# Kernel tuning notes

Hardware: AMD Instinct MI355X
Metric: run time of the kernel (lower is better)

Reference implementation:

```python
import jax, jax.numpy as jnp
import numpy as np

B, N, K, D = 2, 4096, 20, 128
PH = 8          # pos_mlp hidden dim
AH = 4 * D      # attn_mlp hidden dim (attn_mlp_hidden_mult=4)


def setup_inputs() -> dict:
    key = jax.random.key(0)
    ks = jax.random.split(key, 12)
    s = 0.02
    f32 = jnp.float32
    return {
        "x": jax.random.normal(ks[0], (B, N, 3), f32),
        "pos": jax.random.normal(ks[1], (B, N, 3), f32),
        # linear1/2/3 (torch Linear: y = x @ W.T + b)
        "W1": jax.random.normal(ks[2], (D, 3), f32) * s,  "b1": jnp.zeros((D,), f32),
        "W2": jax.random.normal(ks[3], (D, D), f32) * s,  "b2": jnp.zeros((D,), f32),
        "W3": jax.random.normal(ks[4], (D, D), f32) * s,  "b3": jnp.zeros((D,), f32),
        # PointTransformerLayer params
        "Wqkv": jax.random.normal(ks[5], (3 * D, D), f32) * s,          # to_qkv, no bias
        "Wp1": jax.random.normal(ks[6], (PH, 3), f32) * s,  "bp1": jnp.zeros((PH,), f32),
        "Wp2": jax.random.normal(ks[7], (D, PH), f32) * s,  "bp2": jnp.zeros((D,), f32),
        "Wa1": jax.random.normal(ks[8], (AH, D), f32) * s,  "ba1": jnp.zeros((AH,), f32),
        "Wa2": jax.random.normal(ks[9], (D, AH), f32) * s,  "ba2": jnp.zeros((D,), f32),
    }


def reference(x, pos, W1, b1, W2, b2, W3, b3, Wqkv,
              Wp1, bp1, Wp2, bp2, Wa1, ba1, Wa2, ba2):
    h = x @ W1.T + b1            # [B,N,D] linear1
    h1 = h @ W2.T + b2           # [B,N,D] linear2

    # --- PointTransformerLayer (lucidrains, KNN vector attention) ---
    qkv = h1 @ Wqkv.T            # [B,N,3D]
    q, k, v = jnp.split(qkv, 3, axis=-1)

    # squared pairwise distances and K nearest neighbors (self included)
    d2 = jnp.sum((pos[:, :, None, :] - pos[:, None, :, :]) ** 2, axis=-1)  # [B,N,N]
    _, idx = jax.lax.top_k(-d2, K)                                          # [B,N,K]

    gather = jax.vmap(lambda arr, ind: arr[ind])  # per-batch gather -> [B,N,K,*]
    kn = gather(k, idx)          # [B,N,K,D]
    vn = gather(v, idx)          # [B,N,K,D]
    pn = gather(pos, idx)        # [B,N,K,3]

    rel = pos[:, :, None, :] - pn                                   # [B,N,K,3]
    pe = jax.nn.relu(rel @ Wp1.T + bp1) @ Wp2.T + bp2               # pos_mlp [B,N,K,D]

    vn = vn + pe
    sim = jax.nn.relu((q[:, :, None, :] - kn + pe) @ Wa1.T + ba1) @ Wa2.T + ba2  # attn_mlp
    attn = jax.nn.softmax(sim, axis=2)                              # softmax over neighbors
    agg = jnp.sum(attn * vn, axis=2)                                # [B,N,D]

    return h + (agg @ W3.T + b3)  # residual: x + linear3(x1)
```

## Files before the change

kernel.cpp:

```cpp
#include <hip/hip_runtime.h>
#include <stdint.h>

#define BB 2
#define NN 4096
#define KNB 20
#define DD 128
#define PHH 8
#define AHH 512
#define BN (BB*NN)

typedef unsigned short ushort_t;
typedef short bf16x8 __attribute__((ext_vector_type(8)));
typedef float f32x4 __attribute__((ext_vector_type(4)));

__device__ __forceinline__ uint32_t umin32(uint32_t a, uint32_t b) { return a < b ? a : b; }
__device__ __forceinline__ uint32_t umax32(uint32_t a, uint32_t b) { return a > b ? a : b; }

__device__ __forceinline__ ushort_t f2bf(float f) {
    uint32_t x = __float_as_uint(f);
    return (ushort_t)((x + 0x7FFFu + ((x >> 16) & 1u)) >> 16);
}
__device__ __forceinline__ float bf2f(ushort_t u) {
    union { float f; uint32_t i; } c; c.i = ((uint32_t)u) << 16; return c.f;
}

#define SW256(m, byteInRow) ((m)*256 + ((byteInRow) ^ (((m)&7) << 4)))
#define SW128(m, byteInRow) ((m)*128 + ((byteInRow) ^ (((m)&7) << 4)))

__global__ __launch_bounds__(256) void k_prep(
        const float* __restrict__ Wa1, const float* __restrict__ Wa2,
        const float* __restrict__ W2, const float* __restrict__ Wqkv,
        const float* __restrict__ W3, ushort_t* __restrict__ wbf) {
    int i = blockIdx.x*256 + threadIdx.x;
    float v;
    if (i < 65536)        v = Wa1[i];
    else if (i < 131072)  v = Wa2[i - 65536];
    else if (i < 147456)  v = W2[i - 131072];
    else if (i < 196608)  v = Wqkv[i - 147456];
    else                  v = W3[i - 196608];
    wbf[i] = f2bf(v);
}

__global__ __launch_bounds__(256) void k_front(
        const float* __restrict__ x,
        const float* __restrict__ W1, const float* __restrict__ b1,
        const ushort_t* __restrict__ W2bf, const float* __restrict__ b2,
        const ushort_t* __restrict__ Wqkvbf,
        float* __restrict__ h, ushort_t* __restrict__ qf,
        ushort_t* __restrict__ kf, ushort_t* __restrict__ vf) {
    __shared__ __align__(16) char smem[16896];
    float* xs = (float*)(smem + 16384);
    int tid = threadIdx.x, w = tid >> 6, lane = tid & 63;
    int p0 = blockIdx.x * 32;

    if (tid < 96) xs[tid] = x[(size_t)p0*3 + tid];
    __syncthreads();

    #pragma unroll
    for (int it = 0; it < 16; ++it) {
        int lin = it*256 + tid;
        int m = lin >> 7, d = lin & 127;
        float hv = b1[d] + xs[m*3+0]*W1[d*3+0] + xs[m*3+1]*W1[d*3+1] + xs[m*3+2]*W1[d*3+2];
        h[(size_t)(p0+m)*DD + d] = hv;
        *(ushort_t*)&smem[SW256(m, d*2)] = f2bf(hv);
    }
    __syncthreads();

    {
        f32x4 acc[2][2];
        #pragma unroll
        for (int mt = 0; mt < 2; ++mt)
            #pragma unroll
            for (int ntl = 0; ntl < 2; ++ntl) acc[mt][ntl] = (f32x4){0,0,0,0};
        #pragma unroll
        for (int ks = 0; ks < 4; ++ks) {
            int k0 = ks*32 + (lane >> 4)*8;
            bf16x8 aF[2];
            #pragma unroll
            for (int mt = 0; mt < 2; ++mt)
                aF[mt] = *(const bf16x8*)&smem[SW256(mt*16 + (lane & 15), k0*2)];
            #pragma unroll
            for (int ntl = 0; ntl < 2; ++ntl) {
                int n = (2*w + ntl)*16 + (lane & 15);
                bf16x8 bF = *(const bf16x8*)&W2bf[(size_t)n*DD + k0];
                #pragma unroll
                for (int mt = 0; mt < 2; ++mt)
                    acc[mt][ntl] = __builtin_amdgcn_mfma_f32_16x16x32_bf16(aF[mt], bF, acc[mt][ntl], 0, 0, 0);
            }
        }
        #pragma unroll
        for (int ntl = 0; ntl < 2; ++ntl) {
            int n = (2*w + ntl)*16 + (lane & 15);
            float bias = b2[n];
            #pragma unroll
            for (int mt = 0; mt < 2; ++mt)
                #pragma unroll
                for (int i = 0; i < 4; ++i) {
                    int m = mt*16 + (lane >> 4)*4 + i;
                    *(ushort_t*)&smem[8192 + SW256(m, n*2)] = f2bf(acc[mt][ntl][i] + bias);
                }
        }
    }
    __syncthreads();

    {
        f32x4 acc[2][6];
        #pragma unroll
        for (int mt = 0; mt < 2; ++mt)
            #pragma unroll
            for (int ntl = 0; ntl < 6; ++ntl) acc[mt][ntl] = (f32x4){0,0,0,0};
        #pragma unroll
        for (int ks = 0; ks < 4; ++ks) {
            int k0 = ks*32 + (lane >> 4)*8;
            bf16x8 aF[2];
            #pragma unroll
            for (int mt = 0; mt < 2; ++mt)
                aF[mt] = *(const bf16x8*)&smem[8192 + SW256(mt*16 + (lane & 15), k0*2)];
            #pragma unroll
            for (int ntl = 0; ntl < 6; ++ntl) {
                int n = (w*6 + ntl)*16 + (lane & 15);
                bf16x8 bF = *(const bf16x8*)&Wqkvbf[(size_t)n*DD + k0];
                #pragma unroll
                for (int mt = 0; mt < 2; ++mt)
                    acc[mt][ntl] = __builtin_amdgcn_mfma_f32_16x16x32_bf16(aF[mt], bF, acc[mt][ntl], 0, 0, 0);
            }
        }
        #pragma unroll
        for (int ntl = 0; ntl < 6; ++ntl) {
            int n = (w*6 + ntl)*16 + (lane & 15);
            int r = n >> 7, d = n & 127;
            ushort_t* dst = (r == 0) ? qf : (r == 1) ? kf : vf;
            #pragma unroll
            for (int mt = 0; mt < 2; ++mt)
                #pragma unroll
                for (int i = 0; i < 4; ++i) {
                    int m = mt*16 + (lane >> 4)*4 + i;
                    dst[(size_t)(p0+m)*DD + d] = f2bf(acc[mt][ntl][i]);
                }
        }
    }
}

__global__ __launch_bounds__(256) void k_knn(const float* __restrict__ pos, int* __restrict__ idx) {
    int wid  = threadIdx.x >> 6;
    int lane = threadIdx.x & 63;
    int p = blockIdx.x*4 + wid;
    int b = p >> 12;
    float qx = pos[p*3+0], qy = pos[p*3+1], qz = pos[p*3+2];
    const float* pb = pos + (size_t)b*NN*3;

    uint32_t bk[KNB];
    #pragma unroll
    for (int i = 0; i < KNB; ++i) bk[i] = 0xFFFFFFFFu;

    for (int i = 0; i < NN/64; ++i) {
        int j = i*64 + lane;
        float dx = qx - pb[j*3+0];
        float dy = qy - pb[j*3+1];
        float dz = qz - pb[j*3+2];
        float d2 = dx*dx + dy*dy + dz*dz;
        uint32_t key = (__float_as_uint(d2) & 0xFFFFF000u) | (uint32_t)j;
        if (key < bk[KNB-1]) {
            uint32_t c = key;
            #pragma unroll
            for (int t = 0; t < KNB; ++t) {
                uint32_t lo = umin32(c, bk[t]);
                uint32_t hi = umax32(c, bk[t]);
                bk[t] = lo; c = hi;
            }
        }
    }
    for (int r = 0; r < KNB; ++r) {
        uint32_t m = bk[0];
        #pragma unroll
        for (int s = 1; s < 64; s <<= 1)
            m = umin32(m, (uint32_t)__shfl_xor((int)m, s, 64));
        if (lane == 0) idx[(size_t)p*KNB + r] = (int)(m & 0xFFFu);
        bool win = (bk[0] == m);
        #pragma unroll
        for (int t = 0; t < KNB-1; ++t) bk[t] = win ? bk[t+1] : bk[t];
        bk[KNB-1] = win ? 0xFFFFFFFFu : bk[KNB-1];
    }
}

#define XL_OFF 0
#define TL_OFF 20480
#define PH_OFF 30720
#define NIDX_OFF 33280
#define SIM_STRIDE 272

__global__ __launch_bounds__(256, 4) void k_attn(
        const float* __restrict__ pos,
        const ushort_t* __restrict__ qf, const ushort_t* __restrict__ kf,
        const ushort_t* __restrict__ vf, const int* __restrict__ idx,
        const float* __restrict__ Wp1, const float* __restrict__ bp1,
        const float* __restrict__ Wp2, const float* __restrict__ bp2,
        const ushort_t* __restrict__ Wa1bf, const float* __restrict__ ba1,
        const ushort_t* __restrict__ Wa2bf, const float* __restrict__ ba2,
        float* __restrict__ agg) {
    __shared__ __align__(16) char smem[33600];
    float* phv  = (float*)(smem + PH_OFF);
    int*   nidx = (int*)(smem + NIDX_OFF);

    int tid = threadIdx.x, w = tid >> 6, lane = tid & 63;
    int p0 = blockIdx.x * 4, b = p0 >> 12;

    if (tid < 80) nidx[tid] = idx[(size_t)(p0 + tid/20)*KNB + (tid%20)];
    __syncthreads();

    for (int lin = tid; lin < 80*PHH; lin += 256) {
        int m = lin >> 3, jj = lin & 7;
        int g = m / 20;
        int j = nidx[m];
        const float* pq = pos + (size_t)(p0 + g)*3;
        const float* pn = pos + (size_t)(b*NN + j)*3;
        float r0 = pq[0]-pn[0], r1 = pq[1]-pn[1], r2 = pq[2]-pn[2];
        float a = bp1[jj] + r0*Wp1[jj*3+0] + r1*Wp1[jj*3+1] + r2*Wp1[jj*3+2];
        phv[m*PHH + jj] = fmaxf(a, 0.f);
    }
    __syncthreads();

    {
        int d = tid & 127;
        int mpar = tid >> 7;
        float4 wp2a = *(const float4*)(Wp2 + (size_t)d*PHH);
        float4 wp2b = *(const float4*)(Wp2 + (size_t)d*PHH + 4);
        float bp2d = bp2[d];
        float qv[4];
        #pragma unroll
        for (int g = 0; g < 4; ++g) qv[g] = bf2f(qf[(size_t)(p0+g)*DD + d]);
        #pragma unroll
        for (int g = 0; g < 4; ++g) {
            #pragma unroll
            for (int t = 0; t < 10; ++t) {
                int m = g*20 + mpar + 2*t;
                int j = nidx[m];
                float4 pa = *(const float4*)(phv + m*PHH);
                float4 pb = *(const float4*)(phv + m*PHH + 4);
                float pe = bp2d + pa.x*wp2a.x + pa.y*wp2a.y + pa.z*wp2a.z + pa.w*wp2a.w
                                + pb.x*wp2b.x + pb.y*wp2b.y + pb.z*wp2b.z + pb.w*wp2b.w;
                float kv = bf2f(kf[(size_t)(b*NN + j)*DD + d]);
                *(ushort_t*)&smem[XL_OFF + SW256(m, d*2)] = f2bf(qv[g] - kv + pe);
            }
        }
    }
    __syncthreads();

    f32x4 accS[5][2];
    #pragma unroll
    for (int mt = 0; mt < 5; ++mt)
        #pragma unroll
        for (int ntl = 0; ntl < 2; ++ntl) accS[mt][ntl] = (f32x4){0,0,0,0};

    for (int c = 0; c < 8; ++c) {
        f32x4 accB[5];
        #pragma unroll
        for (int mt = 0; mt < 5; ++mt) accB[mt] = (f32x4){0,0,0,0};
        #pragma unroll
        for (int ks = 0; ks < 4; ++ks) {
            int k0 = ks*32 + (lane >> 4)*8;
            bf16x8 aF[5];
            #pragma unroll
            for (int mt = 0; mt < 5; ++mt)
                aF[mt] = *(const bf16x8*)&smem[XL_OFF + SW256(mt*16 + (lane & 15), k0*2)];
            bf16x8 bF = *(const bf16x8*)&Wa1bf[(size_t)(c*64 + w*16 + (lane & 15))*DD + k0];
            #pragma unroll
            for (int mt = 0; mt < 5; ++mt)
                accB[mt] = __builtin_amdgcn_mfma_f32_16x16x32_bf16(aF[mt], bF, accB[mt], 0, 0, 0);
        }
        {
            int al = w*16 + (lane & 15);
            float bias = ba1[c*64 + al];
            #pragma unroll
            for (int mt = 0; mt < 5; ++mt)
                #pragma unroll
                for (int i = 0; i < 4; ++i) {
                    int m = mt*16 + (lane >> 4)*4 + i;
                    *(ushort_t*)&smem[TL_OFF + SW128(m, al*2)] = f2bf(fmaxf(accB[mt][i] + bias, 0.f));
                }
        }
        __syncthreads();

        #pragma unroll
        for (int ks = 0; ks < 2; ++ks) {
            int k0 = ks*32 + (lane >> 4)*8;
            bf16x8 aF[5];
            #pragma unroll
            for (int mt = 0; mt < 5; ++mt)
                aF[mt] = *(const bf16x8*)&smem[TL_OFF + SW128(mt*16 + (lane & 15), k0*2)];
            #pragma unroll
            for (int ntl = 0; ntl < 2; ++ntl) {
                int dd = w*32 + ntl*16 + (lane & 15);
                bf16x8 bF = *(const bf16x8*)&Wa2bf[(size_t)dd*AHH + c*64 + k0];
                #pragma unroll
                for (int mt = 0; mt < 5; ++mt)
                    accS[mt][ntl] = __builtin_amdgcn_mfma_f32_16x16x32_bf16(aF[mt], bF, accS[mt][ntl], 0, 0, 0);
            }
        }
        __syncthreads();
    }

    #pragma unroll
    for (int ntl = 0; ntl < 2; ++ntl) {
        int dd = w*32 + ntl*16 + (lane & 15);
        float bias2 = ba2[dd];
        #pragma unroll
        for (int mt = 0; mt < 5; ++mt)
            #pragma unroll
            for (int i = 0; i < 4; ++i) {
                int m = mt*16 + (lane >> 4)*4 + i;
                *(ushort_t*)&smem[m*SIM_STRIDE + dd*2] = f2bf(accS[mt][ntl][i] + bias2);
            }
    }
    __syncthreads();

    {
        int d = tid & 127;
        int g2 = tid >> 7;
        float4 wp2a = *(const float4*)(Wp2 + (size_t)d*PHH);
        float4 wp2b = *(const float4*)(Wp2 + (size_t)d*PHH + 4);
        float bp2d = bp2[d];
        #pragma unroll
        for (int gi = 0; gi < 2; ++gi) {
            int g = g2 + gi*2;
            float s = 0.f, anum = 0.f;
            #pragma unroll
            for (int kk = 0; kk < KNB; ++kk) {
                int m = g*20 + kk;
                int j = nidx[m];
                float sim = bf2f(*(const ushort_t*)&smem[m*SIM_STRIDE + d*2]);
                float4 pa = *(const float4*)(phv + m*PHH);
                float4 pb = *(const float4*)(phv + m*PHH + 4);
                float pe = bp2d + pa.x*wp2a.x + pa.y*wp2a.y + pa.z*wp2a.z + pa.w*wp2a.w
                                + pb.x*wp2b.x + pb.y*wp2b.y + pb.z*wp2b.z + pb.w*wp2b.w;
                float vv = bf2f(vf[(size_t)(b*NN + j)*DD + d]);
                float e = __expf(sim);
                anum += e * (vv + pe);
                s += e;
            }
            agg[(size_t)(p0 + g)*DD + d] = anum / s;
        }
    }
}

__global__ __launch_bounds__(256) void k_out(
        const float* __restrict__ agg, const float* __restrict__ h,
        const ushort_t* __restrict__ W3bf, const float* __restrict__ b3,
        float* __restrict__ out) {
    __shared__ __align__(16) char smem[8192];
    int tid = threadIdx.x, w = tid >> 6, lane = tid & 63;
    int p0 = blockIdx.x * 32;

    #pragma unroll
    for (int it = 0; it < 16; ++it) {
        int lin = it*256 + tid;
        int m = lin >> 7, d = lin & 127;
        *(ushort_t*)&smem[SW256(m, d*2)] = f2bf(agg[(size_t)(p0+m)*DD + d]);
    }
    __syncthreads();

    f32x4 acc[2][2];
    #pragma unroll
    for (int mt = 0; mt < 2; ++mt)
        #pragma unroll
        for (int ntl = 0; ntl < 2; ++ntl) acc[mt][ntl] = (f32x4){0,0,0,0};
    #pragma unroll
    for (int ks = 0; ks < 4; ++ks) {
        int k0 = ks*32 + (lane >> 4)*8;
        bf16x8 aF[2];
        #pragma unroll
        for (int mt = 0; mt < 2; ++mt)
            aF[mt] = *(const bf16x8*)&smem[SW256(mt*16 + (lane & 15), k0*2)];
        #pragma unroll
        for (int ntl = 0; ntl < 2; ++ntl) {
            int n = (2*w + ntl)*16 + (lane & 15);
            bf16x8 bF = *(const bf16x8*)&W3bf[(size_t)n*DD + k0];
            #pragma unroll
            for (int mt = 0; mt < 2; ++mt)
                acc[mt][ntl] = __builtin_amdgcn_mfma_f32_16x16x32_bf16(aF[mt], bF, acc[mt][ntl], 0, 0, 0);
        }
    }
    #pragma unroll
    for (int ntl = 0; ntl < 2; ++ntl) {
        int n = (2*w + ntl)*16 + (lane & 15);
        float bias = b3[n];
        #pragma unroll
        for (int mt = 0; mt < 2; ++mt)
            #pragma unroll
            for (int i = 0; i < 4; ++i) {
                int m = mt*16 + (lane >> 4)*4 + i;
                size_t o = (size_t)(p0+m)*DD + n;
                out[o] = acc[mt][ntl][i] + bias + h[o];
            }
    }
}

extern "C" void kernel_launch(void* const* d_in, const int* in_sizes, int n_in,
                              void* d_out, int out_size, void* d_ws, size_t ws_size,
                              hipStream_t stream) {
    const float* x    = (const float*)d_in[0];
    const float* pos  = (const float*)d_in[1];
    const float* W1   = (const float*)d_in[2];
    const float* b1   = (const float*)d_in[3];
    const float* W2   = (const float*)d_in[4];
    const float* b2   = (const float*)d_in[5];
    const float* W3   = (const float*)d_in[6];
    const float* b3   = (const float*)d_in[7];
    const float* Wqkv = (const float*)d_in[8];
    const float* Wp1  = (const float*)d_in[9];
    const float* bp1  = (const float*)d_in[10];
    const float* Wp2  = (const float*)d_in[11];
    const float* bp2  = (const float*)d_in[12];
    const float* Wa1  = (const float*)d_in[13];
    const float* ba1  = (const float*)d_in[14];
    const float* Wa2  = (const float*)d_in[15];
    const float* ba2  = (const float*)d_in[16];

    float* ws = (float*)d_ws;
    float* h   = ws;
    float* agg = ws + (size_t)BN*DD;
    ushort_t* qf = (ushort_t*)(ws + 2*(size_t)BN*DD);
    ushort_t* kf = qf + (size_t)BN*DD;
    ushort_t* vf = qf + 2*(size_t)BN*DD;
    int* idx = (int*)((char*)d_ws + 14680064);
    ushort_t* wbf = (ushort_t*)((char*)d_ws + 15335424);
    ushort_t* Wa1bf  = wbf;
    ushort_t* Wa2bf  = wbf + 65536;
    ushort_t* W2bf   = wbf + 131072;
    ushort_t* Wqkvbf = wbf + 147456;
    ushort_t* W3bf   = wbf + 196608;

    k_prep <<<832, 256, 0, stream>>>(Wa1, Wa2, W2, Wqkv, W3, wbf);
    k_front<<<BN/32, 256, 0, stream>>>(x, W1, b1, W2bf, b2, Wqkvbf, h, qf, kf, vf);
    k_knn  <<<BN/4, 256, 0, stream>>>(pos, idx);
    k_attn <<<BN/4, 256, 0, stream>>>(pos, qf, kf, vf, idx,
                                      Wp1, bp1, Wp2, bp2, Wa1bf, ba1, Wa2bf, ba2, agg);
    k_out  <<<BN/32, 256, 0, stream>>>(agg, h, W3bf, b3, (float*)d_out);
}
```

Measured before the change: 179.9 us.

## Merge prep, front and KNN into one launch; restructure attention epilogue with MFMA pos-MLP

Three independent launches (weight cast, front linear layers, KNN) become one kernel that dispatches on block index. Only the large attention weights are still pre-cast to bf16; the small weights are converted on the fly with v_cvt_pk_bf16_f32. In k_attn, the position-MLP second layer now runs on MFMA and v+pe is kept packed in registers. The softmax aggregation is done straight from the MFMA accumulators with cross-lane shuffles, removing the shared-memory sim buffer and an extra barrier. This saves launch gaps and LDS traffic but adds register pressure and bf16 rounding of the positional hidden values.

```diff
diff --git a/kernel.cpp b/kernel.cpp
--- a/kernel.cpp
+++ b/kernel.cpp
@@ -23,171 +23,177 @@
 __device__ __forceinline__ float bf2f(ushort_t u) {
     union { float f; uint32_t i; } c; c.i = ((uint32_t)u) << 16; return c.f;
 }
+__device__ __forceinline__ uint32_t cvt_pk_bf16(float lo, float hi) {
+    uint32_t r;
+    asm("v_cvt_pk_bf16_f32 %0, %1, %2" : "=v"(r) : "v"(lo), "v"(hi));
+    return r;
+}
+__device__ __forceinline__ bf16x8 load_bfrag(const float* __restrict__ src) {
+    float4 x = *(const float4*)src;
+    float4 y = *(const float4*)(src + 4);
+    union { bf16x8 v; uint32_t u[4]; } r;
+    r.u[0] = cvt_pk_bf16(x.x, x.y);
+    r.u[1] = cvt_pk_bf16(x.z, x.w);
+    r.u[2] = cvt_pk_bf16(y.x, y.y);
+    r.u[3] = cvt_pk_bf16(y.z, y.w);
+    return r.v;
+}
 
 #define SW256(m, byteInRow) ((m)*256 + ((byteInRow) ^ (((m)&7) << 4)))
 #define SW128(m, byteInRow) ((m)*128 + ((byteInRow) ^ (((m)&7) << 4)))
 
-__global__ __launch_bounds__(256) void k_prep(
+__global__ __launch_bounds__(256) void k_mega(
+        const float* __restrict__ x, const float* __restrict__ pos,
+        const float* __restrict__ W1, const float* __restrict__ b1,
+        const float* __restrict__ W2f, const float* __restrict__ b2,
+        const float* __restrict__ Wqkvf,
         const float* __restrict__ Wa1, const float* __restrict__ Wa2,
-        const float* __restrict__ W2, const float* __restrict__ Wqkv,
-        const float* __restrict__ W3, ushort_t* __restrict__ wbf) {
-    int i = blockIdx.x*256 + threadIdx.x;
-    float v;
-    if (i < 65536)        v = Wa1[i];
-    else if (i < 131072)  v = Wa2[i - 65536];
-    else if (i < 147456)  v = W2[i - 131072];
-    else if (i < 196608)  v = Wqkv[i - 147456];
-    else                  v = W3[i - 196608];
-    wbf[i] = f2bf(v);
-}
-
-__global__ __launch_bounds__(256) void k_front(
-        const float* __restrict__ x,
-        const float* __restrict__ W1, const float* __restrict__ b1,
-        const ushort_t* __restrict__ W2bf, const float* __restrict__ b2,
-        const ushort_t* __restrict__ Wqkvbf,
         float* __restrict__ h, ushort_t* __restrict__ qf,
-        ushort_t* __restrict__ kf, ushort_t* __restrict__ vf) {
+        ushort_t* __restrict__ kf, ushort_t* __restrict__ vf,
+        int* __restrict__ idx, ushort_t* __restrict__ wbf) {
     __shared__ __align__(16) char smem[16896];
-    float* xs = (float*)(smem + 16384);
     int tid = threadIdx.x, w = tid >> 6, lane = tid & 63;
-    int p0 = blockIdx.x * 32;
-
-    if (tid < 96) xs[tid] = x[(size_t)p0*3 + tid];
-    __syncthreads();
-
-    #pragma unroll
-    for (int it = 0; it < 16; ++it) {
-        int lin = it*256 + tid;
-        int m = lin >> 7, d = lin & 127;
-        float hv = b1[d] + xs[m*3+0]*W1[d*3+0] + xs[m*3+1]*W1[d*3+1] + xs[m*3+2]*W1[d*3+2];
-        h[(size_t)(p0+m)*DD + d] = hv;
-        *(ushort_t*)&smem[SW256(m, d*2)] = f2bf(hv);
-    }
-    __syncthreads();
-
-    {
-        f32x4 acc[2][2];
-        #pragma unroll
-        for (int mt = 0; mt < 2; ++mt)
-            #pragma unroll
-            for (int ntl = 0; ntl < 2; ++ntl) acc[mt][ntl] = (f32x4){0,0,0,0};
-        #pragma unroll
-        for (int ks = 0; ks < 4; ++ks) {
-            int k0 = ks*32 + (lane >> 4)*8;
-            bf16x8 aF[2];
+    int bid = blockIdx.x;
+
+    if (bid < BN/4) {
+        int p = bid*4 + w;
+        int b = p >> 12;
+        float qx = pos[p*3+0], qy = pos[p*3+1], qz = pos[p*3+2];
+        const float* pb = pos + (size_t)b*NN*3;
+        uint32_t bk[KNB];
+        #pragma unroll
+        for (int i = 0; i < KNB; ++i) bk[i] = 0xFFFFFFFFu;
+        for (int i = 0; i < NN/64; ++i) {
+            int j = i*64 + lane;
+            float dx = qx - pb[j*3+0];
+            float dy = qy - pb[j*3+1];
+            float dz = qz - pb[j*3+2];
+            float d2 = dx*dx + dy*dy + dz*dz;
+            uint32_t key = (__float_as_uint(d2) & 0xFFFFF000u) | (uint32_t)j;
+            if (key < bk[KNB-1]) {
+                uint32_t c = key;
+                #pragma unroll
+                for (int t = 0; t < KNB; ++t) {
+                    uint32_t lo = umin32(c, bk[t]);
+                    uint32_t hi = umax32(c, bk[t]);
+                    bk[t] = lo; c = hi;
+                }
+            }
+        }
+        for (int r = 0; r < KNB; ++r) {
+            uint32_t m = bk[0];
+            #pragma unroll
+            for (int s = 1; s < 64; s <<= 1)
+                m = umin32(m, (uint32_t)__shfl_xor((int)m, s, 64));
+            if (lane == 0) idx[(size_t)p*KNB + r] = (int)(m & 0xFFFu);
+            bool win = (bk[0] == m);
+            #pragma unroll
+            for (int t = 0; t < KNB-1; ++t) bk[t] = win ? bk[t+1] : bk[t];
+            bk[KNB-1] = win ? 0xFFFFFFFFu : bk[KNB-1];
+        }
+    } else if (bid < BN/4 + BN/32) {
+        float* xs = (float*)(smem + 16384);
+        int p0 = (bid - BN/4) * 32;
+        if (tid < 96) xs[tid] = x[(size_t)p0*3 + tid];
+        __syncthreads();
+
+        #pragma unroll
+        for (int it = 0; it < 16; ++it) {
+            int lin = it*256 + tid;
+            int m = lin >> 7, d = lin & 127;
+            float hv = b1[d] + xs[m*3+0]*W1[d*3+0] + xs[m*3+1]*W1[d*3+1] + xs[m*3+2]*W1[d*3+2];
+            h[(size_t)(p0+m)*DD + d] = hv;
+            *(ushort_t*)&smem[SW256(m, d*2)] = f2bf(hv);
+        }
+        __syncthreads();
+
+        {
+            f32x4 acc[2][2];
             #pragma unroll
             for (int mt = 0; mt < 2; ++mt)
-                aF[mt] = *(const bf16x8*)&smem[SW256(mt*16 + (lane & 15), k0*2)];
+                #pragma unroll
+                for (int ntl = 0; ntl < 2; ++ntl) acc[mt][ntl] = (f32x4){0,0,0,0};
+            #pragma unroll
+            for (int ks = 0; ks < 4; ++ks) {
+                int k0 = ks*32 + (lane >> 4)*8;
+                bf16x8 aF[2];
+                #pragma unroll
+                for (int mt = 0; mt < 2; ++mt)
+                    aF[mt] = *(const bf16x8*)&smem[SW256(mt*16 + (lane & 15), k0*2)];
+                #pragma unroll
+                for (int ntl = 0; ntl < 2; ++ntl) {
+                    int n = (2*w + ntl)*16 + (lane & 15);
+                    bf16x8 bF = load_bfrag(W2f + (size_t)n*DD + k0);
+                    #pragma unroll
+                    for (int mt = 0; mt < 2; ++mt)
+                        acc[mt][ntl] = __builtin_amdgcn_mfma_f32_16x16x32_bf16(aF[mt], bF, acc[mt][ntl], 0, 0, 0);
+                }
+            }
             #pragma unroll
             for (int ntl = 0; ntl < 2; ++ntl) {
                 int n = (2*w + ntl)*16 + (lane & 15);
-                bf16x8 bF = *(const bf16x8*)&W2bf[(size_t)n*DD + k0];
+                float bias = b2[n];
                 #pragma unroll
                 for (int mt = 0; mt < 2; ++mt)
-                    acc[mt][ntl] = __builtin_amdgcn_mfma_f32_16x16x32_bf16(aF[mt], bF, acc[mt][ntl], 0, 0, 0);
-            }
-        }
-        #pragma unroll
-        for (int ntl = 0; ntl < 2; ++ntl) {
-            int n = (2*w + ntl)*16 + (lane & 15);
-            float bias = b2[n];
+                    #pragma unroll
+                    for (int i = 0; i < 4; ++i) {
+                        int m = mt*16 + (lane >> 4)*4 + i;
+                        *(ushort_t*)&smem[8192 + SW256(m, n*2)] = f2bf(acc[mt][ntl][i] + bias);
+                    }
+            }
+        }
+        __syncthreads();
+
+        {
+            f32x4 acc[2][6];
             #pragma unroll
             for (int mt = 0; mt < 2; ++mt)
                 #pragma unroll
-                for (int i = 0; i < 4; ++i) {
-                    int m = mt*16 + (lane >> 4)*4 + i;
-                    *(ushort_t*)&smem[8192 + SW256(m, n*2)] = f2bf(acc[mt][ntl][i] + bias);
+                for (int ntl = 0; ntl < 6; ++ntl) acc[mt][ntl] = (f32x4){0,0,0,0};
+            #pragma unroll
+            for (int ks = 0; ks < 4; ++ks) {
+                int k0 = ks*32 + (lane >> 4)*8;
+                bf16x8 aF[2];
+                #pragma unroll
+                for (int mt = 0; mt < 2; ++mt)
+                    aF[mt] = *(const bf16x8*)&smem[8192 + SW256(mt*16 + (lane & 15), k0*2)];
+                #pragma unroll
+                for (int ntl = 0; ntl < 6; ++ntl) {
+                    int n = (w*6 + ntl)*16 + (lane & 15);
+                    bf16x8 bF = load_bfrag(Wqkvf + (size_t)n*DD + k0);
+                    #pragma unroll
+                    for (int mt = 0; mt < 2; ++mt)
+                        acc[mt][ntl] = __builtin_amdgcn_mfma_f32_16x16x32_bf16(aF[mt], bF, acc[mt][ntl], 0, 0, 0);
                 }
-        }
-    }
-    __syncthreads();
-
-    {
-        f32x4 acc[2][6];
-        #pragma unroll
-        for (int mt = 0; mt < 2; ++mt)
-            #pragma unroll
-            for (int ntl = 0; ntl < 6; ++ntl) acc[mt][ntl] = (f32x4){0,0,0,0};
-        #pragma unroll
-        for (int ks = 0; ks < 4; ++ks) {
-            int k0 = ks*32 + (lane >> 4)*8;
-            bf16x8 aF[2];
-            #pragma unroll
-            for (int mt = 0; mt < 2; ++mt)
-                aF[mt] = *(const bf16x8*)&smem[8192 + SW256(mt*16 + (lane & 15), k0*2)];
+            }
             #pragma unroll
             for (int ntl = 0; ntl < 6; ++ntl) {
                 int n = (w*6 + ntl)*16 + (lane & 15);
-                bf16x8 bF = *(const bf16x8*)&Wqkvbf[(size_t)n*DD + k0];
+                int r = n >> 7, d = n & 127;
+                ushort_t* dst = (r == 0) ? qf : (r == 1) ? kf : vf;
                 #pragma unroll
                 for (int mt = 0; mt < 2; ++mt)
-                    acc[mt][ntl] = __builtin_amdgcn_mfma_f32_16x16x32_bf16(aF[mt], bF, acc[mt][ntl], 0, 0, 0);
-            }
-        }
-        #pragma unroll
-        for (int ntl = 0; ntl < 6; ++ntl) {
-            int n = (w*6 + ntl)*16 + (lane & 15);
-            int r = n >> 7, d = n & 127;
-            ushort_t* dst = (r == 0) ? qf : (r == 1) ? kf : vf;
-            #pragma unroll
-            for (int mt = 0; mt < 2; ++mt)
-                #pragma unroll
-                for (int i = 0; i < 4; ++i) {
-                    int m = mt*16 + (lane >> 4)*4 + i;
-                    dst[(size_t)(p0+m)*DD + d] = f2bf(acc[mt][ntl][i]);
-                }
-        }
-    }
-}
-
-__global__ __launch_bounds__(256) void k_knn(const float* __restrict__ pos, int* __restrict__ idx) {
-    int wid  = threadIdx.x >> 6;
-    int lane = threadIdx.x & 63;
-    int p = blockIdx.x*4 + wid;
-    int b = p >> 12;
-    float qx = pos[p*3+0], qy = pos[p*3+1], qz = pos[p*3+2];
-    const float* pb = pos + (size_t)b*NN*3;
-
-    uint32_t bk[KNB];
-    #pragma unroll
-    for (int i = 0; i < KNB; ++i) bk[i] = 0xFFFFFFFFu;
-
-    for (int i = 0; i < NN/64; ++i) {
-        int j = i*64 + lane;
-        float dx = qx - pb[j*3+0];
-        float dy = qy - pb[j*3+1];
-        float dz = qz - pb[j*3+2];
-        float d2 = dx*dx + dy*dy + dz*dz;
-        uint32_t key = (__float_as_uint(d2) & 0xFFFFF000u) | (uint32_t)j;
-        if (key < bk[KNB-1]) {
-            uint32_t c = key;
-            #pragma unroll
-            for (int t = 0; t < KNB; ++t) {
-                uint32_t lo = umin32(c, bk[t]);
-                uint32_t hi = umax32(c, bk[t]);
-                bk[t] = lo; c = hi;
-            }
-        }
-    }
-    for (int r = 0; r < KNB; ++r) {
-        uint32_t m = bk[0];
-        #pragma unroll
-        for (int s = 1; s < 64; s <<= 1)
-            m = umin32(m, (uint32_t)__shfl_xor((int)m, s, 64));
-        if (lane == 0) idx[(size_t)p*KNB + r] = (int)(m & 0xFFFu);
-        bool win = (bk[0] == m);
-        #pragma unroll
-        for (int t = 0; t < KNB-1; ++t) bk[t] = win ? bk[t+1] : bk[t];
-        bk[KNB-1] = win ? 0xFFFFFFFFu : bk[KNB-1];
+                    #pragma unroll
+                    for (int i = 0; i < 4; ++i) {
+                        int m = mt*16 + (lane >> 4)*4 + i;
+                        dst[(size_t)(p0+m)*DD + d] = f2bf(acc[mt][ntl][i]);
+                    }
+            }
+        }
+    } else {
+        int base = (bid - (BN/4 + BN/32)) * 2048 + tid * 8;
+        const float* src = (base < 65536) ? (Wa1 + base) : (Wa2 + (base - 65536));
+        union { ushort_t u[8]; uint4 q; } pk;
+        #pragma unroll
+        for (int i = 0; i < 8; ++i) pk.u[i] = f2bf(src[i]);
+        *(uint4*)&wbf[base] = pk.q;
     }
 }
 
 #define XL_OFF 0
 #define TL_OFF 20480
 #define PH_OFF 30720
-#define NIDX_OFF 33280
-#define SIM_STRIDE 272
+#define NIDX_OFF 32000
 
 __global__ __launch_bounds__(256, 4) void k_attn(
         const float* __restrict__ pos,
@@ -198,50 +204,79 @@
         const ushort_t* __restrict__ Wa1bf, const float* __restrict__ ba1,
         const ushort_t* __restrict__ Wa2bf, const float* __restrict__ ba2,
         float* __restrict__ agg) {
-    __shared__ __align__(16) char smem[33600];
-    float* phv  = (float*)(smem + PH_OFF);
-    int*   nidx = (int*)(smem + NIDX_OFF);
+    __shared__ __align__(16) char smem[32320];
+    int* nidx = (int*)(smem + NIDX_OFF);
 
     int tid = threadIdx.x, w = tid >> 6, lane = tid & 63;
+    int lg = lane >> 4, c16 = lane & 15;
     int p0 = blockIdx.x * 4, b = p0 >> 12;
 
     if (tid < 80) nidx[tid] = idx[(size_t)(p0 + tid/20)*KNB + (tid%20)];
     __syncthreads();
 
-    for (int lin = tid; lin < 80*PHH; lin += 256) {
-        int m = lin >> 3, jj = lin & 7;
-        int g = m / 20;
+    if (tid < 80) {
+        int m = tid, g = m / 20;
         int j = nidx[m];
-        const float* pq = pos + (size_t)(p0 + g)*3;
-        const float* pn = pos + (size_t)(b*NN + j)*3;
+        const float* pq = pos + (size_t)(p0+g)*3;
+        const float* pn = pos + (size_t)(b*NN+j)*3;
         float r0 = pq[0]-pn[0], r1 = pq[1]-pn[1], r2 = pq[2]-pn[2];
-        float a = bp1[jj] + r0*Wp1[jj*3+0] + r1*Wp1[jj*3+1] + r2*Wp1[jj*3+2];
-        phv[m*PHH + jj] = fmaxf(a, 0.f);
+        union { ushort_t u[8]; uint4 q; } pk;
+        #pragma unroll
+        for (int jj = 0; jj < PHH; ++jj) {
+            float a = bp1[jj] + r0*Wp1[jj*3+0] + r1*Wp1[jj*3+1] + r2*Wp1[jj*3+2];
+            pk.u[jj] = f2bf(fmaxf(a, 0.f));
+        }
+        *(uint4*)&smem[PH_OFF + m*16] = pk.q;
     }
     __syncthreads();
 
-    {
-        int d = tid & 127;
-        int mpar = tid >> 7;
-        float4 wp2a = *(const float4*)(Wp2 + (size_t)d*PHH);
-        float4 wp2b = *(const float4*)(Wp2 + (size_t)d*PHH + 4);
-        float bp2d = bp2[d];
-        float qv[4];
-        #pragma unroll
-        for (int g = 0; g < 4; ++g) qv[g] = bf2f(qf[(size_t)(p0+g)*DD + d]);
-        #pragma unroll
-        for (int g = 0; g < 4; ++g) {
-            #pragma unroll
-            for (int t = 0; t < 10; ++t) {
-                int m = g*20 + mpar + 2*t;
-                int j = nidx[m];
-                float4 pa = *(const float4*)(phv + m*PHH);
-                float4 pb = *(const float4*)(phv + m*PHH + 4);
-                float pe = bp2d + pa.x*wp2a.x + pa.y*wp2a.y + pa.z*wp2a.z + pa.w*wp2a.w
-                                + pb.x*wp2b.x + pb.y*wp2b.y + pb.z*wp2b.z + pb.w*wp2b.w;
-                float kv = bf2f(kf[(size_t)(b*NN + j)*DD + d]);
-                *(ushort_t*)&smem[XL_OFF + SW256(m, d*2)] = f2bf(qv[g] - kv + pe);
-            }
+    int dA = w*32 + c16, dB = w*32 + 16 + c16;
+    float bp2A = bp2[dA], bp2B = bp2[dB];
+    float ba2A = ba2[dA], ba2B = ba2[dB];
+
+    bf16x8 bP0 = {0,0,0,0,0,0,0,0}, bP1 = {0,0,0,0,0,0,0,0};
+    if (lg == 0) {
+        bP0 = load_bfrag(Wp2 + (size_t)dA*PHH);
+        bP1 = load_bfrag(Wp2 + (size_t)dB*PHH);
+    }
+
+    float qv[4][2];
+    #pragma unroll
+    for (int g = 0; g < 4; ++g) {
+        qv[g][0] = bf2f(qf[(size_t)(p0+g)*DD + dA]);
+        qv[g][1] = bf2f(qf[(size_t)(p0+g)*DD + dB]);
+    }
+
+    uint32_t vpe_pk[5][4];
+
+    #pragma unroll
+    for (int mt = 0; mt < 5; ++mt) {
+        bf16x8 aP = {0,0,0,0,0,0,0,0};
+        if (lg == 0) aP = *(const bf16x8*)&smem[PH_OFF + (mt*16 + c16)*16];
+        f32x4 accP0 = (f32x4){0,0,0,0}, accP1 = (f32x4){0,0,0,0};
+        accP0 = __builtin_amdgcn_mfma_f32_16x16x32_bf16(aP, bP0, accP0, 0, 0, 0);
+        accP1 = __builtin_amdgcn_mfma_f32_16x16x32_bf16(aP, bP1, accP1, 0, 0, 0);
+        float qsA = (mt==0) ? qv[0][0]
+                  : (mt==1) ? (lg>=1 ? qv[1][0] : qv[0][0])
+                  : (mt==2) ? (lg>=2 ? qv[2][0] : qv[1][0])
+                  : (mt==3) ? (lg==3 ? qv[3][0] : qv[2][0])
+                  : qv[3][0];
+        float qsB = (mt==0) ? qv[0][1]
+                  : (mt==1) ? (lg>=1 ? qv[1][1] : qv[0][1])
+                  : (mt==2) ? (lg>=2 ? qv[2][1] : qv[1][1])
+                  : (mt==3) ? (lg==3 ? qv[3][1] : qv[2][1])
+                  : qv[3][1];
+        #pragma unroll
+        for (int i = 0; i < 4; ++i) {
+            int m = mt*16 + lg*4 + i;
+            int j = nidx[m];
+            const ushort_t* kr = kf + (size_t)(b*NN+j)*DD;
+            const ushort_t* vr = vf + (size_t)(b*NN+j)*DD;
+            float peA = accP0[i] + bp2A;
+            float peB = accP1[i] + bp2B;
+            *(ushort_t*)&smem[XL_OFF + SW256(m, dA*2)] = f2bf(qsA - bf2f(kr[dA]) + peA);
+            *(ushort_t*)&smem[XL_OFF + SW256(m, dB*2)] = f2bf(qsB - bf2f(kr[dB]) + peB);
+            vpe_pk[mt][i] = cvt_pk_bf16(bf2f(vr[dA]) + peA, bf2f(vr[dB]) + peB);
         }
     }
     __syncthreads();
@@ -258,24 +293,24 @@
         for (int mt = 0; mt < 5; ++mt) accB[mt] = (f32x4){0,0,0,0};
         #pragma unroll
         for (int ks = 0; ks < 4; ++ks) {
-            int k0 = ks*32 + (lane >> 4)*8;
+            int k0 = ks*32 + lg*8;
             bf16x8 aF[5];
             #pragma unroll
             for (int mt = 0; mt < 5; ++mt)
-                aF[mt] = *(const bf16x8*)&smem[XL_OFF + SW256(mt*16 + (lane & 15), k0*2)];
-            bf16x8 bF = *(const bf16x8*)&Wa1bf[(size_t)(c*64 + w*16 + (lane & 15))*DD + k0];
+                aF[mt] = *(const bf16x8*)&smem[XL_OFF + SW256(mt*16 + c16, k0*2)];
+            bf16x8 bF = *(const bf16x8*)&Wa1bf[(size_t)(c*64 + w*16 + c16)*DD + k0];
             #pragma unroll
             for (int mt = 0; mt < 5; ++mt)
                 accB[mt] = __builtin_amdgcn_mfma_f32_16x16x32_bf16(aF[mt], bF, accB[mt], 0, 0, 0);
         }
         {
-            int al = w*16 + (lane & 15);
+            int al = w*16 + c16;
             float bias = ba1[c*64 + al];
             #pragma unroll
             for (int mt = 0; mt < 5; ++mt)
                 #pragma unroll
                 for (int i = 0; i < 4; ++i) {
-                    int m = mt*16 + (lane >> 4)*4 + i;
+                    int m = mt*16 + lg*4 + i;
                     *(ushort_t*)&smem[TL_OFF + SW128(m, al*2)] = f2bf(fmaxf(accB[mt][i] + bias, 0.f));
                 }
         }
@@ -283,14 +318,14 @@
 
         #pragma unroll
         for (int ks = 0; ks < 2; ++ks) {
-            int k0 = ks*32 + (lane >> 4)*8;
+            int k0 = ks*32 + lg*8;
             bf16x8 aF[5];
             #pragma unroll
             for (int mt = 0; mt < 5; ++mt)
-                aF[mt] = *(const bf16x8*)&smem[TL_OFF + SW128(mt*16 + (lane & 15), k0*2)];
+                aF[mt] = *(const bf16x8*)&smem[TL_OFF + SW128(mt*16 + c16, k0*2)];
             #pragma unroll
             for (int ntl = 0; ntl < 2; ++ntl) {
-                int dd = w*32 + ntl*16 + (lane & 15);
+                int dd = w*32 + ntl*16 + c16;
                 bf16x8 bF = *(const bf16x8*)&Wa2bf[(size_t)dd*AHH + c*64 + k0];
                 #pragma unroll
                 for (int mt = 0; mt < 5; ++mt)
@@ -300,52 +335,58 @@
         __syncthreads();
     }
 
-    #pragma unroll
-    for (int ntl = 0; ntl < 2; ++ntl) {
-        int dd = w*32 + ntl*16 + (lane & 15);
-        float bias2 = ba2[dd];
-        #pragma unroll
-        for (int mt = 0; mt < 5; ++mt)
-            #pragma unroll
-            for (int i = 0; i < 4; ++i) {
-                int m = mt*16 + (lane >> 4)*4 + i;
-                *(ushort_t*)&smem[m*SIM_STRIDE + dd*2] = f2bf(accS[mt][ntl][i] + bias2);
-            }
-    }
-    __syncthreads();
-
-    {
-        int d = tid & 127;
-        int g2 = tid >> 7;
-        float4 wp2a = *(const float4*)(Wp2 + (size_t)d*PHH);
-        float4 wp2b = *(const float4*)(Wp2 + (size_t)d*PHH + 4);
-        float bp2d = bp2[d];
-        #pragma unroll
-        for (int gi = 0; gi < 2; ++gi) {
-            int g = g2 + gi*2;
-            float s = 0.f, anum = 0.f;
-            #pragma unroll
-            for (int kk = 0; kk < KNB; ++kk) {
-                int m = g*20 + kk;
-                int j = nidx[m];
-                float sim = bf2f(*(const ushort_t*)&smem[m*SIM_STRIDE + d*2]);
-                float4 pa = *(const float4*)(phv + m*PHH);
-                float4 pb = *(const float4*)(phv + m*PHH + 4);
-                float pe = bp2d + pa.x*wp2a.x + pa.y*wp2a.y + pa.z*wp2a.z + pa.w*wp2a.w
-                                + pb.x*wp2b.x + pb.y*wp2b.y + pb.z*wp2b.z + pb.w*wp2b.w;
-                float vv = bf2f(vf[(size_t)(b*NN + j)*DD + d]);
-                float e = __expf(sim);
-                anum += e * (vv + pe);
-                s += e;
-            }
-            agg[(size_t)(p0 + g)*DD + d] = anum / s;
-        }
-    }
+    float s_mtA[5], a_mtA[5], s_mtB[5], a_mtB[5];
+    #pragma unroll
+    for (int mt = 0; mt < 5; ++mt) {
+        float sa = 0.f, aa = 0.f, sb = 0.f, ab = 0.f;
+        #pragma unroll
+        for (int i = 0; i < 4; ++i) {
+            float eA = __expf(accS[mt][0][i] + ba2A);
+            float eB = __expf(accS[mt][1][i] + ba2B);
+            uint32_t pk = vpe_pk[mt][i];
+            float vA = bf2f((ushort_t)(pk & 0xFFFFu));
+            float vB = bf2f((ushort_t)(pk >> 16));
+            sa += eA; aa += eA*vA;
+            sb += eB; ab += eB*vB;
+        }
+        s_mtA[mt] = sa; a_mtA[mt] = aa; s_mtB[mt] = sb; a_mtB[mt] = ab;
+    }
+    bool eq0 = (lg==0), ge1 = (lg>=1), ge2 = (lg>=2), le1 = (lg<=1), le2 = (lg<=2), eq3 = (lg==3);
+    float s0A = s_mtA[0] + (eq0 ? s_mtA[1] : 0.f);
+    float s1A = (ge1 ? s_mtA[1] : 0.f) + (le1 ? s_mtA[2] : 0.f);
+    float s2A = (ge2 ? s_mtA[2] : 0.f) + (le2 ? s_mtA[3] : 0.f);
+    float s3A = (eq3 ? s_mtA[3] : 0.f) + s_mtA[4];
+    float a0A = a_mtA[0] + (eq0 ? a_mtA[1] : 0.f);
+    float a1A = (ge1 ? a_mtA[1] : 0.f) + (le1 ? a_mtA[2] : 0.f);
+    float a2A = (ge2 ? a_mtA[2] : 0.f) + (le2 ? a_mtA[3] : 0.f);
+    float a3A = (eq3 ? a_mtA[3] : 0.f) + a_mtA[4];
+    float s0B = s_mtB[0] + (eq0 ? s_mtB[1] : 0.f);
+    float s1B = (ge1 ? s_mtB[1] : 0.f) + (le1 ? s_mtB[2] : 0.f);
+    float s2B = (ge2 ? s_mtB[2] : 0.f) + (le2 ? s_mtB[3] : 0.f);
+    float s3B = (eq3 ? s_mtB[3] : 0.f) + s_mtB[4];
+    float a0B = a_mtB[0] + (eq0 ? a_mtB[1] : 0.f);
+    float a1B = (ge1 ? a_mtB[1] : 0.f) + (le1 ? a_mtB[2] : 0.f);
+    float a2B = (ge2 ? a_mtB[2] : 0.f) + (le2 ? a_mtB[3] : 0.f);
+    float a3B = (eq3 ? a_mtB[3] : 0.f) + a_mtB[4];
+
+    #define RED2(v) { v += __shfl_xor(v, 16, 64); v += __shfl_xor(v, 32, 64); }
+    RED2(s0A) RED2(s1A) RED2(s2A) RED2(s3A)
+    RED2(a0A) RED2(a1A) RED2(a2A) RED2(a3A)
+    RED2(s0B) RED2(s1B) RED2(s2B) RED2(s3B)
+    RED2(a0B) RED2(a1B) RED2(a2B) RED2(a3B)
+    #undef RED2
+
+    float myS_A = (lg==0) ? s0A : (lg==1) ? s1A : (lg==2) ? s2A : s3A;
+    float myA_A = (lg==0) ? a0A : (lg==1) ? a1A : (lg==2) ? a2A : a3A;
+    float myS_B = (lg==0) ? s0B : (lg==1) ? s1B : (lg==2) ? s2B : s3B;
+    float myA_B = (lg==0) ? a0B : (lg==1) ? a1B : (lg==2) ? a2B : a3B;
+    agg[(size_t)(p0+lg)*DD + dA] = myA_A / myS_A;
+    agg[(size_t)(p0+lg)*DD + dB] = myA_B / myS_B;
 }
 
 __global__ __launch_bounds__(256) void k_out(
         const float* __restrict__ agg, const float* __restrict__ h,
-        const ushort_t* __restrict__ W3bf, const float* __restrict__ b3,
+        const float* __restrict__ W3f, const float* __restrict__ b3,
         float* __restrict__ out) {
     __shared__ __align__(16) char smem[8192];
     int tid = threadIdx.x, w = tid >> 6, lane = tid & 63;
@@ -374,7 +415,7 @@
         #pragma unroll
         for (int ntl = 0; ntl < 2; ++ntl) {
             int n = (2*w + ntl)*16 + (lane & 15);
-            bf16x8 bF = *(const bf16x8*)&W3bf[(size_t)n*DD + k0];
+            bf16x8 bF = load_bfrag(W3f + (size_t)n*DD + k0);
             #pragma unroll
             for (int mt = 0; mt < 2; ++mt)
                 acc[mt][ntl] = __builtin_amdgcn_mfma_f32_16x16x32_bf16(aF[mt], bF, acc[mt][ntl], 0, 0, 0);
@@ -424,16 +465,12 @@
     ushort_t* vf = qf + 2*(size_t)BN*DD;
     int* idx = (int*)((char*)d_ws + 14680064);
     ushort_t* wbf = (ushort_t*)((char*)d_ws + 15335424);
-    ushort_t* Wa1bf  = wbf;
-    ushort_t* Wa2bf  = wbf + 65536;
-    ushort_t* W2bf   = wbf + 131072;
-    ushort_t* Wqkvbf = wbf + 147456;
-    ushort_t* W3bf   = wbf + 196608;
-
-    k_prep <<<832, 256, 0, stream>>>(Wa1, Wa2, W2, Wqkv, W3, wbf);
-    k_front<<<BN/32, 256, 0, stream>>>(x, W1, b1, W2bf, b2, Wqkvbf, h, qf, kf, vf);
-    k_knn  <<<BN/4, 256, 0, stream>>>(pos, idx);
-    k_attn <<<BN/4, 256, 0, stream>>>(pos, qf, kf, vf, idx,
-                                      Wp1, bp1, Wp2, bp2, Wa1bf, ba1, Wa2bf, ba2, agg);
-    k_out  <<<BN/32, 256, 0, stream>>>(agg, h, W3bf, b3, (float*)d_out);
-}
+    ushort_t* Wa1bf = wbf;
+    ushort_t* Wa2bf = wbf + 65536;
+
+    k_mega<<<BN/4 + BN/32 + 64, 256, 0, stream>>>(x, pos, W1, b1, W2, b2, Wqkv,
+                                                  Wa1, Wa2, h, qf, kf, vf, idx, wbf);
+    k_attn<<<BN/4, 256, 0, stream>>>(pos, qf, kf, vf, idx,
+                                     Wp1, bp1, Wp2, bp2, Wa1bf, ba1, Wa2bf, ba2, agg);
+    k_out <<<BN/32, 256, 0, stream>>>(agg, h, W3, b3, (float*)d_out);
+}
```

Measured after the change: 175.1 us. -2.6%, faster.
